# Kernel optimization log

Hardware: AMD Instinct MI355X
Metric: run time of the kernel (lower is better)

The kernel has to match this reference:

```python
import jax, jax.numpy as jnp
import numpy as np

N = 20000
DEG = 16
E = N * DEG
IN_DIM = 512
OUT_DIM = 512
H = 4
D = OUT_DIM // H            # head_dim = 128
POS_DIM = 3
M_ROPE = D // (POS_DIM * 2) # 21
D_ROPE = POS_DIM * 2 * M_ROPE  # 126 (2 trailing dims unrotated)
ROPE_BASE = 10000.0

INV_FREQ = jnp.exp(-jnp.arange(M_ROPE, dtype=jnp.float32) * (np.log(ROPE_BASE) / M_ROPE))


def _rope(t, pos):
    # t: (N, D, H), pos: (N, POS_DIM)
    n = t.shape[0]
    angles = pos[:, :, None] * INV_FREQ[None, None, :]        # (N, POS_DIM, M)
    cos = jnp.cos(angles)[..., None]                           # (N, POS_DIM, M, 1)
    sin = jnp.sin(angles)[..., None]
    part = t[:, :D_ROPE, :].reshape(n, POS_DIM, M_ROPE, 2, H)
    even, odd = part[..., 0, :], part[..., 1, :]
    rot_even = even * cos - odd * sin
    rot_odd = even * sin + odd * cos
    rot = jnp.stack((rot_even, rot_odd), axis=3).reshape(n, D_ROPE, H)
    return jnp.concatenate([rot, t[:, D_ROPE:, :]], axis=1)


def setup_inputs() -> dict:
    key = jax.random.key(0)
    ks = jax.random.split(key, 12)
    x = jax.random.normal(ks[0], (N, IN_DIM), jnp.float32)
    pos = jax.random.uniform(ks[1], (N, POS_DIM), jnp.float32) * 100.0
    rows = jnp.repeat(jnp.arange(N, dtype=jnp.int32), DEG)  # sorted, every node has DEG out-edges
    cols = jax.random.randint(ks[2], (E,), 0, N, dtype=jnp.int32)
    s = 1.0 / np.sqrt(IN_DIM)
    Wq = jax.random.normal(ks[3], (OUT_DIM, IN_DIM), jnp.float32) * s
    Wk = jax.random.normal(ks[4], (OUT_DIM, IN_DIM), jnp.float32) * s
    Wv = jax.random.normal(ks[5], (OUT_DIM, IN_DIM), jnp.float32) * s
    Wo = jax.random.normal(ks[6], (OUT_DIM, OUT_DIM), jnp.float32) * s
    bq = jax.random.normal(ks[7], (OUT_DIM,), jnp.float32) * 0.01
    bk = jax.random.normal(ks[8], (OUT_DIM,), jnp.float32) * 0.01
    bv = jax.random.normal(ks[9], (OUT_DIM,), jnp.float32) * 0.01
    bo = jax.random.normal(ks[10], (OUT_DIM,), jnp.float32) * 0.01
    return {"x": x, "pos": pos, "rows": rows, "cols": cols,
            "Wq": Wq, "bq": bq, "Wk": Wk, "bk": bk, "Wv": Wv, "bv": bv, "Wo": Wo, "bo": bo}


def reference(x, pos, rows, cols, Wq, bq, Wk, bk, Wv, bv, Wo, bo):
    n = x.shape[0]
    q = (x @ Wq.T + bq).reshape(n, D, H)
    k = (x @ Wk.T + bk).reshape(n, D, H)
    v = (x @ Wv.T + bv).reshape(n, D, H)
    # scaling by sqrt(k.size(1)) == sqrt(head_dim)
    q = q / jnp.sqrt(jnp.asarray(D, q.dtype))
    q = _rope(q, pos)
    k = _rope(k, pos)
    # per-edge scores: s[e,h] = sum_d q[rows[e],d,h] * k[cols[e],d,h]
    scores = jnp.einsum('edh,edh->eh', q[rows], k[cols])  # (E, H)
    # row-wise sparse softmax per head
    row_max = jax.ops.segment_max(scores, rows, num_segments=n, indices_are_sorted=True)
    p = jnp.exp(scores - row_max[rows])
    denom = jax.ops.segment_sum(p, rows, num_segments=n, indices_are_sorted=True)
    attn = p / denom[rows]                                 # (E, H)
    # bspmm: y[i,d,h] = sum_{e: rows[e]=i} attn[e,h] * v[cols[e],d,h]
    y = jax.ops.segment_sum(attn[:, None, :] * v[cols], rows, num_segments=n, indices_are_sorted=True)
    out = y.reshape(n, OUT_DIM) @ Wo.T + bo
    return out
```

## Files before the change

kernel.cpp:

```cpp
#include <hip/hip_runtime.h>
#include <hip/hip_bf16.h>

#define NN 20000
#define DEG 16
#define KD 512
#define OD 512
#define NH 4
#define DH 128
#define DROPE 126

#define BM 128
#define BN 128
#define BK 64

typedef unsigned short u16;
typedef unsigned int u32;
typedef __attribute__((ext_vector_type(8))) short short8;
typedef __attribute__((ext_vector_type(4))) float f32x4;

__device__ __forceinline__ float b2f(u16 u){ return __uint_as_float((u32)u << 16); }
__device__ __forceinline__ u16 f2b(float f){
  u32 x = __float_as_uint(f);
  return (u16)((x + 0x7fffu + ((x >> 16) & 1u)) >> 16);
}
__device__ __forceinline__ void up8(uint4 u, float* f){
  f[0]=__uint_as_float(u.x<<16); f[1]=__uint_as_float(u.x&0xffff0000u);
  f[2]=__uint_as_float(u.y<<16); f[3]=__uint_as_float(u.y&0xffff0000u);
  f[4]=__uint_as_float(u.z<<16); f[5]=__uint_as_float(u.z&0xffff0000u);
  f[6]=__uint_as_float(u.w<<16); f[7]=__uint_as_float(u.w&0xffff0000u);
}
__device__ __forceinline__ uint4 cvt8(const float* s){
  uint4 a = *(const uint4*)s;
  uint4 b = *(const uint4*)(s + 4);
  uint4 o;
  o.x = (u32)f2b(__uint_as_float(a.x)) | ((u32)f2b(__uint_as_float(a.y)) << 16);
  o.y = (u32)f2b(__uint_as_float(a.z)) | ((u32)f2b(__uint_as_float(a.w)) << 16);
  o.z = (u32)f2b(__uint_as_float(b.x)) | ((u32)f2b(__uint_as_float(b.y)) << 16);
  o.w = (u32)f2b(__uint_as_float(b.z)) | ((u32)f2b(__uint_as_float(b.w)) << 16);
  return o;
}

__device__ __forceinline__ void load_lds16(const u16* g, u16* l) {
  __builtin_amdgcn_global_load_lds(
      (const __attribute__((address_space(1))) void*)g,
      (__attribute__((address_space(3))) void*)l, 16, 0, 0);
}

struct ConvJob {
  const float* x;  u16* xb;
  const float* w[4]; u16* wb[4];
  const float* b[4]; u16* bb[4];
};
__global__ __launch_bounds__(256) void conv_all(ConvJob j) {
  const int b = blockIdx.x;
  if (b < 5000) {
    const int i8 = (b * 256 + threadIdx.x) * 8;
    *(uint4*)(j.xb + i8) = cvt8(j.x + i8);
  } else if (b < 5512) {
    const int t = b - 5000;
    const int wsel = t >> 7;
    const int i8 = ((t & 127) * 256 + threadIdx.x) * 8;
    if (wsel < 3) {
      *(uint4*)(j.wb[wsel] + i8) = cvt8(j.w[wsel] + i8);
    } else {
      const int o = i8 >> 9, cp = i8 & 511;
      const int h = cp >> 7, d0 = cp & 127;
      const float* src = j.w[3] + (size_t)o * 512 + h;
      float tmp[8];
      #pragma unroll
      for (int t2 = 0; t2 < 8; t2++) tmp[t2] = src[(size_t)(d0 + t2) * 4];
      uint4 ov;
      ov.x = (u32)f2b(tmp[0]) | ((u32)f2b(tmp[1]) << 16);
      ov.y = (u32)f2b(tmp[2]) | ((u32)f2b(tmp[3]) << 16);
      ov.z = (u32)f2b(tmp[4]) | ((u32)f2b(tmp[5]) << 16);
      ov.w = (u32)f2b(tmp[6]) | ((u32)f2b(tmp[7]) << 16);
      *(uint4*)(j.wb[3] + i8) = ov;
    }
  } else {
    const int vsel = threadIdx.x >> 6;
    const int i8 = (threadIdx.x & 63) * 8;
    *(uint4*)(j.bb[vsel] + i8) = cvt8(j.b[vsel] + i8);
  }
}

__global__ __launch_bounds__(256, 4) void gemm_k(
    const u16* __restrict__ A,
    const u16* __restrict__ W0, const u16* __restrict__ B0,
    const u16* __restrict__ W1, const u16* __restrict__ B1,
    const u16* __restrict__ W2, const u16* __restrict__ B2,
    const float* __restrict__ pos,
    u16* __restrict__ o0, u16* __restrict__ o1, void* __restrict__ o2,
    int M, int only2, int f32out)
{
  __shared__ __align__(16) char smem[36864];
  __shared__ float posS[BM*3];
  __shared__ float freqS[21];
  u16* As = (u16*)smem;
  u16* Bs = As + BM*BK;

  const int b = blockIdx.x;
  const int xcd = b & 7, rem = b >> 3;
  int rowT, colT, w;
  if (only2) {
    rowT = (rem >> 2)*8 + xcd; colT = rem & 3; w = 2;
  } else {
    rowT = (rem / 12)*8 + xcd; const int sub = rem % 12; colT = sub & 3; w = sub >> 2;
  }
  if (rowT*BM >= M) return;

  const int tid = threadIdx.x;
  const int wave = tid >> 6, lane = tid & 63;
  const int wr = wave >> 1, wc = wave & 1;
  const int lm = lane & 15, lq = lane >> 4;
  const u16* W  = (w == 0) ? W0 : ((w == 1) ? W1 : W2);
  const u16* Bi = (w == 0) ? B0 : ((w == 1) ? B1 : B2);
  const int emode = only2 ? 3 : w;
  u16* outQKV = (w == 0) ? o0 : ((w == 1) ? o1 : (u16*)o2);

  f32x4 acc[4][4];
  #pragma unroll
  for (int i = 0; i < 4; i++)
    #pragma unroll
    for (int jj = 0; jj < 4; jj++)
      acc[i][jj] = (f32x4){0.f, 0.f, 0.f, 0.f};

  if (emode < 2) {
    if (tid < BM) {
      int gr = rowT*BM + tid; if (gr >= M) gr = M - 1;
      posS[tid*3+0] = pos[gr*3+0];
      posS[tid*3+1] = pos[gr*3+1];
      posS[tid*3+2] = pos[gr*3+2];
    }
    if (tid >= BM && tid < BM + 21)
      freqS[tid - BM] = __expf(-(float)(tid - BM) * 0.43858763676077064f);
  }

  for (int kt = 0; kt < KD; kt += BK) {
    #pragma unroll
    for (int it = 0; it < 4; it++) {
      const int chunk = it*256 + wave*64 + lane;
      const int row = chunk >> 3, gseg = (chunk & 7) ^ (row & 7);
      int gr = rowT*BM + row; if (gr >= M) gr = M - 1;
      load_lds16(A + (size_t)gr*KD + kt + gseg*8,
                 As + (size_t)(it*256 + wave*64)*8);
    }
    #pragma unroll
    for (int it = 0; it < 4; it++) {
      const int chunk = it*256 + wave*64 + lane;
      const int row = chunk >> 3, gseg = (chunk & 7) ^ (row & 7);
      load_lds16(W + (size_t)(colT*BN + row)*KD + kt + gseg*8,
                 Bs + (size_t)(it*256 + wave*64)*8);
    }
    __syncthreads();
    #pragma unroll
    for (int kk = 0; kk < BK; kk += 32) {
      const int ks = kk >> 3;
      short8 af[4], bfr[4];
      #pragma unroll
      for (int i = 0; i < 4; i++) {
        const int ra = wr*64 + i*16 + lm;
        af[i] = *(const short8*)(As + (size_t)(ra*8 + ((ks + lq) ^ (ra & 7)))*8);
      }
      #pragma unroll
      for (int i = 0; i < 4; i++) {
        const int rb = wc*64 + i*16 + lm;
        bfr[i] = *(const short8*)(Bs + (size_t)(rb*8 + ((ks + lq) ^ (rb & 7)))*8);
      }
      #pragma unroll
      for (int mi = 0; mi < 4; mi++)
        #pragma unroll
        for (int ni = 0; ni < 4; ni++)
          acc[mi][ni] = __builtin_amdgcn_mfma_f32_16x16x32_bf16(af[mi], bfr[ni], acc[mi][ni], 0, 0, 0);
    }
    __syncthreads();
  }

  float bvv[4];
  #pragma unroll
  for (int ni = 0; ni < 4; ni++)
    bvv[ni] = b2f(Bi[colT*BN + wc*64 + ni*16 + lm]);

  u16* Cs = (u16*)smem;

  if (emode == 3) {
    #pragma unroll
    for (int mi = 0; mi < 4; mi++)
      #pragma unroll
      for (int ni = 0; ni < 4; ni++) {
        const int Cg = colT*BN + wc*64 + ni*16 + lm;
        #pragma unroll
        for (int r = 0; r < 4; r++) {
          const int grow = rowT*BM + wr*64 + mi*16 + lq*4 + r;
          if (grow < M) ((float*)o2)[(size_t)grow*OD + Cg] = acc[mi][ni][r] + bvv[ni];
        }
      }
    return;
  }

  #pragma unroll
  for (int mi = 0; mi < 4; mi++) {
    #pragma unroll
    for (int ni = 0; ni < 4; ni++) {
      const int cloc = wc*64 + ni*16 + lm;
      const int h = cloc & 3, dloc = cloc >> 2;
      const int d = colT*32 + dloc;
      #pragma unroll
      for (int r = 0; r < 4; r++) {
        const int rloc = wr*64 + mi*16 + lq*4 + r;
        float v = acc[mi][ni][r] + bvv[ni];
        if (emode == 0) v *= 0.08838834764831845f;
        float vr = v;
        if (emode < 2) {
          const float partner = __shfl_xor(v, 4);
          if (d < DROPE) {
            const int pp = d / 42, rem2 = d - pp*42, m = rem2 >> 1, par = rem2 & 1;
            const float ang = posS[rloc*3 + pp] * freqS[m];
            float sn, cs; __sincosf(ang, &sn, &cs);
            vr = par ? (v*cs + partner*sn) : (v*cs - partner*sn);
          }
        }
        Cs[rloc*144 + h*36 + dloc] = f2b(vr);
      }
    }
  }
  __syncthreads();
  #pragma unroll
  for (int pass = 0; pass < 8; pass++) {
    const int c2 = pass*256 + tid;
    const int dd8 = c2 & 3, h = (c2 >> 2) & 3, rloc = c2 >> 4;
    const int grow = rowT*BM + rloc;
    if (grow < M) {
      uint2 a = *(const uint2*)(Cs + rloc*144 + h*36 + dd8*8);
      uint2 b2 = *(const uint2*)(Cs + rloc*144 + h*36 + dd8*8 + 4);
      *(uint4*)(outQKV + ((size_t)grow*NH + h)*DH + colT*32 + dd8*8)
          = make_uint4(a.x, a.y, b2.x, b2.y);
    }
  }
}

__global__ __launch_bounds__(256, 3) void edge_attn(
    const int* __restrict__ cols, const u16* __restrict__ qf,
    const u16* __restrict__ kf, const u16* __restrict__ vf,
    u16* __restrict__ y)
{
  const int b = blockIdx.x;
  const int xcd = b & 7;
  const int head = xcd >> 1;
  const int nbase = (b >> 3) * 32 + (xcd & 1) * 16;
  const int wave = threadIdx.x >> 6, lane = threadIdx.x & 63;
  const int g = lane >> 4, l16 = lane & 15;
  const int n = nbase + wave*4 + g;

  const int col = cols[n*DEG + l16];
  const uint4 qv = *(const uint4*)(qf + ((size_t)n*NH + head)*DH + l16*8);

  uint4 kreg[16];
  #pragma unroll
  for (int jj = 0; jj < 16; jj++) {
    const int cj = __shfl(col, g*16 + jj);
    kreg[jj] = *(const uint4*)(kf + ((size_t)cj*NH + head)*DH + l16*8);
  }
  float qa[8]; up8(qv, qa);

  float s = 0.f;
  #pragma unroll
  for (int jj = 0; jj < 16; jj++) {
    float ka[8]; up8(kreg[jj], ka);
    float pr = qa[0]*ka[0] + qa[1]*ka[1] + qa[2]*ka[2] + qa[3]*ka[3]
             + qa[4]*ka[4] + qa[5]*ka[5] + qa[6]*ka[6] + qa[7]*ka[7];
    pr += __shfl_xor(pr, 1);
    pr += __shfl_xor(pr, 2);
    pr += __shfl_xor(pr, 4);
    pr += __shfl_xor(pr, 8);
    s = (l16 == jj) ? pr : s;
  }

  float mx = s;
  #pragma unroll
  for (int msk = 1; msk < 16; msk <<= 1) mx = fmaxf(mx, __shfl_xor(mx, msk));
  float p = expf(s - mx);
  float dn = p;
  #pragma unroll
  for (int msk = 1; msk < 16; msk <<= 1) dn += __shfl_xor(dn, msk);
  const float attn = p / dn;

  uint4 vreg[16];
  #pragma unroll
  for (int jj = 0; jj < 16; jj++) {
    const int cj = __shfl(col, g*16 + jj);
    vreg[jj] = *(const uint4*)(vf + ((size_t)cj*NH + head)*DH + l16*8);
  }
  float ya[8];
  #pragma unroll
  for (int t = 0; t < 8; t++) ya[t] = 0.f;
  #pragma unroll
  for (int jj = 0; jj < 16; jj++) {
    const float a = __shfl(attn, g*16 + jj);
    float va[8]; up8(vreg[jj], va);
    #pragma unroll
    for (int t = 0; t < 8; t++) ya[t] += a*va[t];
  }
  u32 pk[4];
  #pragma unroll
  for (int t = 0; t < 4; t++)
    pk[t] = (u32)f2b(ya[2*t]) | ((u32)f2b(ya[2*t+1]) << 16);
  *(uint4*)(y + ((size_t)n*NH + head)*DH + l16*8) = make_uint4(pk[0], pk[1], pk[2], pk[3]);
}

extern "C" void kernel_launch(void* const* d_in, const int* in_sizes, int n_in,
                              void* d_out, int out_size, void* d_ws, size_t ws_size,
                              hipStream_t stream) {
  (void)in_sizes; (void)n_in; (void)out_size; (void)ws_size;
  const float* x   = (const float*)d_in[0];
  const float* pos = (const float*)d_in[1];
  const int* cols = (const int*)d_in[3];
  const float* Wq = (const float*)d_in[4];
  const float* bq = (const float*)d_in[5];
  const float* Wk = (const float*)d_in[6];
  const float* bk = (const float*)d_in[7];
  const float* Wv = (const float*)d_in[8];
  const float* bv = (const float*)d_in[9];
  const float* Wo = (const float*)d_in[10];
  const float* bo = (const float*)d_in[11];

  char* ws = (char*)d_ws;
  size_t off = 0;
  auto carve = [&](size_t bytes) { char* p = ws + off; off += (bytes + 15) & ~(size_t)15; return p; };
  u16* xb   = (u16*)carve((size_t)NN*KD*2);
  u16* Wqb  = (u16*)carve((size_t)OD*KD*2);
  u16* Wkb  = (u16*)carve((size_t)OD*KD*2);
  u16* Wvb  = (u16*)carve((size_t)OD*KD*2);
  u16* Wob  = (u16*)carve((size_t)OD*OD*2);
  u16* bqb  = (u16*)carve((size_t)OD*2);
  u16* bkb  = (u16*)carve((size_t)OD*2);
  u16* bvb  = (u16*)carve((size_t)OD*2);
  u16* bob  = (u16*)carve((size_t)OD*2);
  u16* qf   = (u16*)carve((size_t)NN*OD*2);
  u16* kf   = (u16*)carve((size_t)NN*OD*2);
  u16* vf   = (u16*)carve((size_t)NN*OD*2);
  u16* y    = (u16*)carve((size_t)NN*OD*2);

  ConvJob cj;
  cj.x = x; cj.xb = xb;
  cj.w[0]=Wq; cj.w[1]=Wk; cj.w[2]=Wv; cj.w[3]=Wo;
  cj.wb[0]=Wqb; cj.wb[1]=Wkb; cj.wb[2]=Wvb; cj.wb[3]=Wob;
  cj.b[0]=bq; cj.b[1]=bk; cj.b[2]=bv; cj.b[3]=bo;
  cj.bb[0]=bqb; cj.bb[1]=bkb; cj.bb[2]=bvb; cj.bb[3]=bob;
  conv_all<<<dim3(5513), 256, 0, stream>>>(cj);

  gemm_k<<<dim3(1920), 256, 0, stream>>>(xb, Wqb, bqb, Wkb, bkb, Wvb, bvb, pos,
                                         qf, kf, (void*)vf, NN, 0, 0);
  edge_attn<<<dim3(5000), 256, 0, stream>>>(cols, qf, kf, vf, y);
  gemm_k<<<dim3(640), 256, 0, stream>>>(y, Wqb, bqb, Wkb, bkb, Wob, bob, pos,
                                        qf, kf, d_out, NN, 1, 1);
}
```

Measured before the change: 245.2 us.

## Double-buffer LDS tiles in QKV/output GEMM to overlap loads with MFMA

Splits shared memory into two buffers and prefetches the next K-tile with direct-to-LDS loads while MFMAs run on the current one, using explicit vmcnt waits and raw barriers. This is meant to hide global-load latency that the single-buffer loop exposed at every K step. LDS use rises to 64 KB per block and the launch bound drops from 4 to 2 blocks per CU, so occupancy-based latency hiding is reduced. Correctness depends on the hand-counted vmcnt(8) matching the eight outstanding loads per stage.

```diff
diff --git a/kernel.cpp b/kernel.cpp
--- a/kernel.cpp
+++ b/kernel.cpp
@@ -83,7 +83,7 @@
   }
 }
 
-__global__ __launch_bounds__(256, 4) void gemm_k(
+__global__ __launch_bounds__(256, 2) void gemm_k(
     const u16* __restrict__ A,
     const u16* __restrict__ W0, const u16* __restrict__ B0,
     const u16* __restrict__ W1, const u16* __restrict__ B1,
@@ -92,11 +92,9 @@
     u16* __restrict__ o0, u16* __restrict__ o1, void* __restrict__ o2,
     int M, int only2, int f32out)
 {
-  __shared__ __align__(16) char smem[36864];
+  __shared__ __align__(16) char smem[65536];
   __shared__ float posS[BM*3];
   __shared__ float freqS[21];
-  u16* As = (u16*)smem;
-  u16* Bs = As + BM*BK;
 
   const int b = blockIdx.x;
   const int xcd = b & 7, rem = b >> 3;
@@ -134,24 +132,42 @@
     if (tid >= BM && tid < BM + 21)
       freqS[tid - BM] = __expf(-(float)(tid - BM) * 0.43858763676077064f);
   }
-
-  for (int kt = 0; kt < KD; kt += BK) {
+  __builtin_amdgcn_sched_barrier(0);
+  asm volatile("s_waitcnt vmcnt(0)" ::: "memory");
+
+  auto stage = [&](int bufi, int kt) {
+    u16* Asb = (u16*)(smem + bufi*32768);
+    u16* Bsb = Asb + BM*BK;
     #pragma unroll
     for (int it = 0; it < 4; it++) {
       const int chunk = it*256 + wave*64 + lane;
       const int row = chunk >> 3, gseg = (chunk & 7) ^ (row & 7);
       int gr = rowT*BM + row; if (gr >= M) gr = M - 1;
       load_lds16(A + (size_t)gr*KD + kt + gseg*8,
-                 As + (size_t)(it*256 + wave*64)*8);
+                 Asb + (size_t)(it*256 + wave*64)*8);
     }
     #pragma unroll
     for (int it = 0; it < 4; it++) {
       const int chunk = it*256 + wave*64 + lane;
       const int row = chunk >> 3, gseg = (chunk & 7) ^ (row & 7);
       load_lds16(W + (size_t)(colT*BN + row)*KD + kt + gseg*8,
-                 Bs + (size_t)(it*256 + wave*64)*8);
-    }
-    __syncthreads();
+                 Bsb + (size_t)(it*256 + wave*64)*8);
+    }
+  };
+
+  stage(0, 0);
+
+  for (int t = 0; t < 8; t++) {
+    const int cur = t & 1;
+    if (t < 7) stage(cur ^ 1, (t + 1) * BK);
+    __builtin_amdgcn_sched_barrier(0);
+    if (t < 7) asm volatile("s_waitcnt vmcnt(8)" ::: "memory");
+    else       asm volatile("s_waitcnt vmcnt(0)" ::: "memory");
+    __builtin_amdgcn_s_barrier();
+    __builtin_amdgcn_sched_barrier(0);
+
+    const u16* Asb = (const u16*)(smem + cur*32768);
+    const u16* Bsb = Asb + BM*BK;
     #pragma unroll
     for (int kk = 0; kk < BK; kk += 32) {
       const int ks = kk >> 3;
@@ -159,12 +175,12 @@
       #pragma unroll
       for (int i = 0; i < 4; i++) {
         const int ra = wr*64 + i*16 + lm;
-        af[i] = *(const short8*)(As + (size_t)(ra*8 + ((ks + lq) ^ (ra & 7)))*8);
+        af[i] = *(const short8*)(Asb + (size_t)(ra*8 + ((ks + lq) ^ (ra & 7)))*8);
       }
       #pragma unroll
       for (int i = 0; i < 4; i++) {
         const int rb = wc*64 + i*16 + lm;
-        bfr[i] = *(const short8*)(Bs + (size_t)(rb*8 + ((ks + lq) ^ (rb & 7)))*8);
+        bfr[i] = *(const short8*)(Bsb + (size_t)(rb*8 + ((ks + lq) ^ (rb & 7)))*8);
       }
       #pragma unroll
       for (int mi = 0; mi < 4; mi++)
@@ -172,7 +188,8 @@
         for (int ni = 0; ni < 4; ni++)
           acc[mi][ni] = __builtin_amdgcn_mfma_f32_16x16x32_bf16(af[mi], bfr[ni], acc[mi][ni], 0, 0, 0);
     }
-    __syncthreads();
+    __builtin_amdgcn_sched_barrier(0);
+    __builtin_amdgcn_s_barrier();
   }
 
   float bvv[4];
```

New measurement: 258.3 us. +5.3%, slower.
